# Kernel tuning notes

Hardware: AMD Instinct MI355X
Metric: run time of the kernel (lower is better)

Reference implementation:

```python
import jax, jax.numpy as jnp
import numpy as np

K_SIZE = 3
CH_IN = 256
NFILT = 256

def setup_inputs() -> dict:
    key = jax.random.key(0)
    k1, k2 = jax.random.split(key)
    x = jax.random.normal(k1, (32, 56, 56, CH_IN), dtype=jnp.float32)
    stdv = 1.0 / np.sqrt(K_SIZE * K_SIZE * CH_IN)
    w = jax.random.normal(k2, (K_SIZE, K_SIZE, CH_IN, NFILT), dtype=jnp.float32) * stdv
    pruning_mask = jnp.ones((K_SIZE * K_SIZE * CH_IN, NFILT), dtype=jnp.float32)
    return {"x": x, "w": w, "pruning_mask": pruning_mask}

def _magnitude_aware_weight(w):
    # scale = mean |w| over (kh, kw, cin), per output filter; stop-gradient
    scale = jax.lax.stop_gradient(jnp.mean(jnp.abs(w), axis=(0, 1, 2), keepdims=True))
    bw_no_grad = scale * jnp.sign(w)
    clipped = jnp.clip(w, -1.0, 1.0)
    # STE: forward = scale*sign(w), backward = d(clip(w,-1,1))
    return jax.lax.stop_gradient(bw_no_grad) - jax.lax.stop_gradient(clipped) + clipped

def reference(x, w, pruning_mask):
    kernel = _magnitude_aware_weight(w) * pruning_mask.reshape(K_SIZE, K_SIZE, CH_IN, NFILT)
    out = jax.lax.conv_general_dilated(
        x, kernel,
        window_strides=(1, 1),
        padding="SAME",
        dimension_numbers=("NHWC", "HWIO", "NHWC"),
    )
    return out
```

## Files before the change

### kernel.cpp

```cpp
#include <hip/hip_runtime.h>

typedef unsigned short u16;
typedef u16 u16x8 __attribute__((ext_vector_type(8)));
typedef __bf16 bf16x8 __attribute__((ext_vector_type(8)));
typedef float f32x4 __attribute__((ext_vector_type(4)));

#define NPIX 100352
#define KTOT 2304

static __device__ __forceinline__ u16 f2bf(float f) {
  unsigned u = __float_as_uint(f);
  return (u16)((u + 0x7fffu + ((u >> 16) & 1u)) >> 16);
}

static __device__ __forceinline__ bf16x8 as_bf(u16x8 v) {
  union { u16x8 u; bf16x8 b; } t; t.u = v; return t.b;
}

__global__ void scale_accum_k(const float* __restrict__ w, float* __restrict__ scale) {
  const int t = threadIdx.x;
  const long b = blockIdx.x;
  const float* p = w + b * 256 * 256 + t;
  float acc = 0.f;
#pragma unroll 8
  for (int e = 0; e < 256; ++e) acc += fabsf(p[(long)e * 256]);
  atomicAdd(&scale[t], acc);
}

__global__ void pack_w_k(const float* __restrict__ w, const float* __restrict__ mask,
                         const float* __restrict__ ssum, u16* __restrict__ wp) {
  __shared__ u16 t[128][33];
  const int k0 = blockIdx.x * 32;
  const int f0 = blockIdx.y * 128;
  const int tid = threadIdx.x;
#pragma unroll
  for (int i = 0; i < 16; ++i) {
    int idx = tid + i * 256;
    int kk = idx >> 7;
    int ff = idx & 127;
    long g = (long)(k0 + kk) * 256 + f0 + ff;
    float wv = w[g];
    float mv = mask[g];
    float sc = ssum[f0 + ff] * (1.0f / 2304.0f);
    float sg = (wv > 0.f) ? 1.f : ((wv < 0.f) ? -1.f : 0.f);
    t[ff][kk] = f2bf(sc * sg * mv);
  }
  __syncthreads();
#pragma unroll
  for (int i = 0; i < 8; ++i) {
    int idx = tid + i * 256;
    int row = idx >> 4;
    int c = idx & 15;
    unsigned v = (unsigned)t[row][2 * c] | ((unsigned)t[row][2 * c + 1] << 16);
    *(unsigned*)(wp + (long)(f0 + row) * KTOT + k0 + 2 * c) = v;
  }
}

__global__ void cvt_x_k(const float* __restrict__ x, u16* __restrict__ xb) {
  const long i = ((long)blockIdx.x * 256 + threadIdx.x) * 8;
  float4 a = *(const float4*)(x + i);
  float4 b = *(const float4*)(x + i + 4);
  u16x8 r;
  r[0] = f2bf(a.x); r[1] = f2bf(a.y); r[2] = f2bf(a.z); r[3] = f2bf(a.w);
  r[4] = f2bf(b.x); r[5] = f2bf(b.y); r[6] = f2bf(b.z); r[7] = f2bf(b.w);
  *(u16x8*)(xb + i) = r;
}

template <bool XB>
__global__ __launch_bounds__(256) void conv_gemm_k(
    const float* __restrict__ x, const u16* __restrict__ xb,
    const u16* __restrict__ wp, float* __restrict__ out) {
  __shared__ u16 As[128 * 40];
  __shared__ u16 Bs[128 * 40];

  const int tid = threadIdx.x;
  const int m0 = blockIdx.x * 128;
  const int n0 = blockIdx.y * 128;

  const int cc = tid & 3;
  const int r0 = tid >> 2;
  const int gm0 = m0 + r0;
  const int gm1 = gm0 + 64;
  const int pix0 = gm0 % 3136, oh0 = pix0 / 56, ow0 = pix0 % 56;
  const int pix1 = gm1 % 3136, oh1 = pix1 / 56, ow1 = pix1 % 56;

  const int lane = tid & 63;
  const int wv = tid >> 6;
  const int wm = wv & 1, wn = wv >> 1;
  const int lm = lane & 15, kq = lane >> 4;
  const int aoff = (wm * 64 + lm) * 40 + kq * 8;
  const int boff = (wn * 64 + lm) * 40 + kq * 8;

  u16* as0 = As + r0 * 40 + cc * 8;
  u16* as1 = As + (r0 + 64) * 40 + cc * 8;
  u16* bs0 = Bs + r0 * 40 + cc * 8;
  u16* bs1 = Bs + (r0 + 64) * 40 + cc * 8;

  const u16* wr0 = wp + (long)(n0 + r0) * KTOT + cc * 8;
  const u16* wr1 = wr0 + (long)64 * KTOT;

  f32x4 acc[4][4] = {};

  for (int khw = 0; khw < 9; ++khw) {
    const int dh = khw / 3 - 1;
    const int dw = khw % 3 - 1;
    const bool v0 = ((unsigned)(oh0 + dh) < 56u) && ((unsigned)(ow0 + dw) < 56u);
    const bool v1 = ((unsigned)(oh1 + dh) < 56u) && ((unsigned)(ow1 + dw) < 56u);
    const long p0 = ((long)gm0 + dh * 56 + dw) * 256 + cc * 8;
    const long p1 = ((long)gm1 + dh * 56 + dw) * 256 + cc * 8;
    const u16* wk0 = wr0 + khw * 256;
    const u16* wk1 = wr1 + khw * 256;

    for (int ct = 0; ct < 8; ++ct) {
      const int ci0 = ct * 32;
      u16x8 a0 = {0, 0, 0, 0, 0, 0, 0, 0};
      u16x8 a1 = {0, 0, 0, 0, 0, 0, 0, 0};
      if (XB) {
        if (v0) a0 = *(const u16x8*)(xb + p0 + ci0);
        if (v1) a1 = *(const u16x8*)(xb + p1 + ci0);
      } else {
        float4 l0 = make_float4(0, 0, 0, 0), h0 = make_float4(0, 0, 0, 0);
        float4 l1 = make_float4(0, 0, 0, 0), h1 = make_float4(0, 0, 0, 0);
        if (v0) { l0 = *(const float4*)(x + p0 + ci0); h0 = *(const float4*)(x + p0 + ci0 + 4); }
        if (v1) { l1 = *(const float4*)(x + p1 + ci0); h1 = *(const float4*)(x + p1 + ci0 + 4); }
        a0[0] = f2bf(l0.x); a0[1] = f2bf(l0.y); a0[2] = f2bf(l0.z); a0[3] = f2bf(l0.w);
        a0[4] = f2bf(h0.x); a0[5] = f2bf(h0.y); a0[6] = f2bf(h0.z); a0[7] = f2bf(h0.w);
        a1[0] = f2bf(l1.x); a1[1] = f2bf(l1.y); a1[2] = f2bf(l1.z); a1[3] = f2bf(l1.w);
        a1[4] = f2bf(h1.x); a1[5] = f2bf(h1.y); a1[6] = f2bf(h1.z); a1[7] = f2bf(h1.w);
      }
      u16x8 b0 = *(const u16x8*)(wk0 + ci0);
      u16x8 b1 = *(const u16x8*)(wk1 + ci0);

      __syncthreads();
      *(u16x8*)as0 = a0;
      *(u16x8*)as1 = a1;
      *(u16x8*)bs0 = b0;
      *(u16x8*)bs1 = b1;
      __syncthreads();

      bf16x8 av[4], bv[4];
#pragma unroll
      for (int i = 0; i < 4; ++i) av[i] = *(const bf16x8*)(As + aoff + i * 640);
#pragma unroll
      for (int i = 0; i < 4; ++i) bv[i] = *(const bf16x8*)(Bs + boff + i * 640);
#pragma unroll
      for (int mi = 0; mi < 4; ++mi) {
#pragma unroll
        for (int ni = 0; ni < 4; ++ni) {
          acc[mi][ni] = __builtin_amdgcn_mfma_f32_16x16x32_bf16(av[mi], bv[ni], acc[mi][ni], 0, 0, 0);
        }
      }
    }
  }

  float* op = out + (long)(m0 + wm * 64 + kq * 4) * 256 + n0 + wn * 64 + lm;
#pragma unroll
  for (int mi = 0; mi < 4; ++mi) {
#pragma unroll
    for (int ni = 0; ni < 4; ++ni) {
      float* p = op + (long)mi * 16 * 256 + ni * 16;
      f32x4 v = acc[mi][ni];
      p[0] = v[0];
      p[256] = v[1];
      p[512] = v[2];
      p[768] = v[3];
    }
  }
}

extern "C" void kernel_launch(void* const* d_in, const int* in_sizes, int n_in,
                              void* d_out, int out_size, void* d_ws, size_t ws_size,
                              hipStream_t stream) {
  const float* x = (const float*)d_in[0];
  const float* w = (const float*)d_in[1];
  const float* mask = (const float*)d_in[2];
  float* out = (float*)d_out;

  float* scale = (float*)d_ws;
  u16* wp = (u16*)((char*)d_ws + 1088);
  u16* xb = (u16*)((char*)d_ws + 1088 + 1179648);
  const size_t need = 1088 + 1179648 + (size_t)NPIX * 256 * 2;

  hipMemsetAsync(d_ws, 0, 1088, stream);
  scale_accum_k<<<9, 256, 0, stream>>>(w, scale);
  pack_w_k<<<dim3(72, 2), 256, 0, stream>>>(w, mask, scale, wp);
  if (ws_size >= need) {
    cvt_x_k<<<NPIX * 256 / (256 * 8), 256, 0, stream>>>(x, xb);
    conv_gemm_k<true><<<dim3(784, 2), 256, 0, stream>>>(x, xb, wp, out);
  } else {
    conv_gemm_k<false><<<dim3(784, 2), 256, 0, stream>>>(x, xb, wp, out);
  }
}
```

Baseline: 416.1 us.

## Pad input spatially and stream tiles into LDS with direct global-to-LDS loads

Converts the input to bf16 inside a zero-padded 58x58 per-image buffer, so the conv GEMM needs no boundary checks. The main kernel now uses global_load_lds to copy A and B tiles straight into LDS, with an XOR-swizzled unpadded layout to avoid bank conflicts, which removes the register round-trip. The weight-scale reduction is spread over more blocks. In exchange it adds a full memset of the padded buffer plus a scatter kernel, and relies on the 16-byte direct LDS load path and a larger workspace.

```diff
diff --git a/kernel.cpp b/kernel.cpp
--- a/kernel.cpp
+++ b/kernel.cpp
@@ -7,23 +7,25 @@
 
 #define NPIX 100352
 #define KTOT 2304
+#define IMG_PAD (58 * 58 * 256)
 
 static __device__ __forceinline__ u16 f2bf(float f) {
   unsigned u = __float_as_uint(f);
   return (u16)((u + 0x7fffu + ((u >> 16) & 1u)) >> 16);
 }
 
-static __device__ __forceinline__ bf16x8 as_bf(u16x8 v) {
-  union { u16x8 u; bf16x8 b; } t; t.u = v; return t.b;
+static __device__ __forceinline__ void gld_lds16(const u16* g, u16* l) {
+  __builtin_amdgcn_global_load_lds(
+      (const __attribute__((address_space(1))) void*)g,
+      (__attribute__((address_space(3))) void*)l, 16, 0, 0);
 }
 
 __global__ void scale_accum_k(const float* __restrict__ w, float* __restrict__ scale) {
   const int t = threadIdx.x;
-  const long b = blockIdx.x;
-  const float* p = w + b * 256 * 256 + t;
+  const float* p = w + (long)blockIdx.x * 64 * 256 + t;
   float acc = 0.f;
-#pragma unroll 8
-  for (int e = 0; e < 256; ++e) acc += fabsf(p[(long)e * 256]);
+#pragma unroll
+  for (int e = 0; e < 64; ++e) acc += fabsf(p[(long)e * 256]);
   atomicAdd(&scale[t], acc);
 }
 
@@ -56,51 +58,127 @@
   }
 }
 
-__global__ void cvt_x_k(const float* __restrict__ x, u16* __restrict__ xb) {
-  const long i = ((long)blockIdx.x * 256 + threadIdx.x) * 8;
-  float4 a = *(const float4*)(x + i);
-  float4 b = *(const float4*)(x + i + 4);
-  u16x8 r;
-  r[0] = f2bf(a.x); r[1] = f2bf(a.y); r[2] = f2bf(a.z); r[3] = f2bf(a.w);
-  r[4] = f2bf(b.x); r[5] = f2bf(b.y); r[6] = f2bf(b.z); r[7] = f2bf(b.w);
-  *(u16x8*)(xb + i) = r;
-}
-
-template <bool XB>
-__global__ __launch_bounds__(256) void conv_gemm_k(
-    const float* __restrict__ x, const u16* __restrict__ xb,
-    const u16* __restrict__ wp, float* __restrict__ out) {
+__global__ void fill_xpad_k(const float* __restrict__ x, u16* __restrict__ xp) {
+  const int tid = threadIdx.x;
+  const int pix = blockIdx.x * 8 + (tid >> 5);
+  const int c0 = (tid & 31) * 8;
+  const int img = pix / 3136;
+  const int r = pix % 3136;
+  const int oh = r / 56, ow = r % 56;
+  const float* s = x + (long)pix * 256 + c0;
+  float4 a = *(const float4*)s;
+  float4 b = *(const float4*)(s + 4);
+  u16x8 v;
+  v[0] = f2bf(a.x); v[1] = f2bf(a.y); v[2] = f2bf(a.z); v[3] = f2bf(a.w);
+  v[4] = f2bf(b.x); v[5] = f2bf(b.y); v[6] = f2bf(b.z); v[7] = f2bf(b.w);
+  *(u16x8*)(xp + (long)img * IMG_PAD + ((oh + 1) * 58 + ow + 1) * 256 + c0) = v;
+}
+
+__global__ __launch_bounds__(256) void conv_gemm2_k(
+    const u16* __restrict__ xpad, const u16* __restrict__ wp, float* __restrict__ out) {
+  __shared__ u16 As[128 * 32];
+  __shared__ u16 Bs[128 * 32];
+
+  const int tid = threadIdx.x;
+  const int lane = tid & 63;
+  const int wv = tid >> 6;
+  const int m0 = blockIdx.x * 128;
+  const int n0 = blockIdx.y * 128;
+
+  const int srow = lane >> 2;
+  const int cg = (lane & 3) ^ (srow & 3);
+  const int r0 = wv * 32 + srow;
+  const int r1 = r0 + 16;
+
+  const int gm0 = m0 + r0, gm1 = m0 + r1;
+  const int i0 = gm0 / 3136, q0 = gm0 % 3136;
+  const int i1 = gm1 / 3136, q1 = gm1 % 3136;
+  const u16* ap0 = xpad + (long)i0 * IMG_PAD + ((q0 / 56 + 1) * 58 + (q0 % 56) + 1) * 256 + cg * 8;
+  const u16* ap1 = xpad + (long)i1 * IMG_PAD + ((q1 / 56 + 1) * 58 + (q1 % 56) + 1) * 256 + cg * 8;
+  const u16* bp0 = wp + (long)(n0 + r0) * KTOT + cg * 8;
+  const u16* bp1 = wp + (long)(n0 + r1) * KTOT + cg * 8;
+
+  u16* asw0 = As + wv * 1024;
+  u16* asw1 = As + wv * 1024 + 512;
+  u16* bsw0 = Bs + wv * 1024;
+  u16* bsw1 = Bs + wv * 1024 + 512;
+
+  const int wm = wv & 1, wn = wv >> 1;
+  const int lm = lane & 15, kq = lane >> 4;
+  const int aoff = (wm * 64 + lm) * 32 + (kq ^ (lm & 3)) * 8;
+  const int boff = (wn * 64 + lm) * 32 + (kq ^ (lm & 3)) * 8;
+
+  f32x4 acc[4][4] = {};
+
+  for (int khw = 0; khw < 9; ++khw) {
+    const int dh = khw / 3 - 1, dw = khw % 3 - 1;
+    const int d = (dh * 58 + dw) * 256;
+    const u16* a0 = ap0 + d;
+    const u16* a1 = ap1 + d;
+    const u16* b0 = bp0 + khw * 256;
+    const u16* b1 = bp1 + khw * 256;
+#pragma unroll
+    for (int ct = 0; ct < 8; ++ct) {
+      gld_lds16(a0 + ct * 32, asw0);
+      gld_lds16(a1 + ct * 32, asw1);
+      gld_lds16(b0 + ct * 32, bsw0);
+      gld_lds16(b1 + ct * 32, bsw1);
+      __syncthreads();
+      bf16x8 av[4], bv[4];
+#pragma unroll
+      for (int i = 0; i < 4; ++i) av[i] = *(const bf16x8*)(As + aoff + i * 512);
+#pragma unroll
+      for (int i = 0; i < 4; ++i) bv[i] = *(const bf16x8*)(Bs + boff + i * 512);
+#pragma unroll
+      for (int mi = 0; mi < 4; ++mi)
+#pragma unroll
+        for (int ni = 0; ni < 4; ++ni)
+          acc[mi][ni] = __builtin_amdgcn_mfma_f32_16x16x32_bf16(av[mi], bv[ni], acc[mi][ni], 0, 0, 0);
+      __syncthreads();
+    }
+  }
+
+  float* op = out + (long)(m0 + wm * 64 + kq * 4) * 256 + n0 + wn * 64 + lm;
+#pragma unroll
+  for (int mi = 0; mi < 4; ++mi) {
+#pragma unroll
+    for (int ni = 0; ni < 4; ++ni) {
+      float* p = op + (long)mi * 16 * 256 + ni * 16;
+      f32x4 v = acc[mi][ni];
+      p[0] = v[0];
+      p[256] = v[1];
+      p[512] = v[2];
+      p[768] = v[3];
+    }
+  }
+}
+
+__global__ __launch_bounds__(256) void conv_gemm_fb_k(
+    const float* __restrict__ x, const u16* __restrict__ wp, float* __restrict__ out) {
   __shared__ u16 As[128 * 40];
   __shared__ u16 Bs[128 * 40];
-
   const int tid = threadIdx.x;
   const int m0 = blockIdx.x * 128;
   const int n0 = blockIdx.y * 128;
-
   const int cc = tid & 3;
   const int r0 = tid >> 2;
   const int gm0 = m0 + r0;
   const int gm1 = gm0 + 64;
   const int pix0 = gm0 % 3136, oh0 = pix0 / 56, ow0 = pix0 % 56;
   const int pix1 = gm1 % 3136, oh1 = pix1 / 56, ow1 = pix1 % 56;
-
   const int lane = tid & 63;
   const int wv = tid >> 6;
   const int wm = wv & 1, wn = wv >> 1;
   const int lm = lane & 15, kq = lane >> 4;
   const int aoff = (wm * 64 + lm) * 40 + kq * 8;
   const int boff = (wn * 64 + lm) * 40 + kq * 8;
-
   u16* as0 = As + r0 * 40 + cc * 8;
   u16* as1 = As + (r0 + 64) * 40 + cc * 8;
   u16* bs0 = Bs + r0 * 40 + cc * 8;
   u16* bs1 = Bs + (r0 + 64) * 40 + cc * 8;
-
   const u16* wr0 = wp + (long)(n0 + r0) * KTOT + cc * 8;
   const u16* wr1 = wr0 + (long)64 * KTOT;
-
   f32x4 acc[4][4] = {};
-
   for (int khw = 0; khw < 9; ++khw) {
     const int dh = khw / 3 - 1;
     const int dw = khw % 3 - 1;
@@ -110,62 +188,44 @@
     const long p1 = ((long)gm1 + dh * 56 + dw) * 256 + cc * 8;
     const u16* wk0 = wr0 + khw * 256;
     const u16* wk1 = wr1 + khw * 256;
-
     for (int ct = 0; ct < 8; ++ct) {
       const int ci0 = ct * 32;
-      u16x8 a0 = {0, 0, 0, 0, 0, 0, 0, 0};
-      u16x8 a1 = {0, 0, 0, 0, 0, 0, 0, 0};
-      if (XB) {
-        if (v0) a0 = *(const u16x8*)(xb + p0 + ci0);
-        if (v1) a1 = *(const u16x8*)(xb + p1 + ci0);
-      } else {
-        float4 l0 = make_float4(0, 0, 0, 0), h0 = make_float4(0, 0, 0, 0);
-        float4 l1 = make_float4(0, 0, 0, 0), h1 = make_float4(0, 0, 0, 0);
-        if (v0) { l0 = *(const float4*)(x + p0 + ci0); h0 = *(const float4*)(x + p0 + ci0 + 4); }
-        if (v1) { l1 = *(const float4*)(x + p1 + ci0); h1 = *(const float4*)(x + p1 + ci0 + 4); }
-        a0[0] = f2bf(l0.x); a0[1] = f2bf(l0.y); a0[2] = f2bf(l0.z); a0[3] = f2bf(l0.w);
-        a0[4] = f2bf(h0.x); a0[5] = f2bf(h0.y); a0[6] = f2bf(h0.z); a0[7] = f2bf(h0.w);
-        a1[0] = f2bf(l1.x); a1[1] = f2bf(l1.y); a1[2] = f2bf(l1.z); a1[3] = f2bf(l1.w);
-        a1[4] = f2bf(h1.x); a1[5] = f2bf(h1.y); a1[6] = f2bf(h1.z); a1[7] = f2bf(h1.w);
-      }
+      u16x8 a0 = {0,0,0,0,0,0,0,0}, a1 = {0,0,0,0,0,0,0,0};
+      float4 l0 = make_float4(0,0,0,0), h0 = make_float4(0,0,0,0);
+      float4 l1 = make_float4(0,0,0,0), h1 = make_float4(0,0,0,0);
+      if (v0) { l0 = *(const float4*)(x + p0 + ci0); h0 = *(const float4*)(x + p0 + ci0 + 4); }
+      if (v1) { l1 = *(const float4*)(x + p1 + ci0); h1 = *(const float4*)(x + p1 + ci0 + 4); }
+      a0[0]=f2bf(l0.x); a0[1]=f2bf(l0.y); a0[2]=f2bf(l0.z); a0[3]=f2bf(l0.w);
+      a0[4]=f2bf(h0.x); a0[5]=f2bf(h0.y); a0[6]=f2bf(h0.z); a0[7]=f2bf(h0.w);
+      a1[0]=f2bf(l1.x); a1[1]=f2bf(l1.y); a1[2]=f2bf(l1.z); a1[3]=f2bf(l1.w);
+      a1[4]=f2bf(h1.x); a1[5]=f2bf(h1.y); a1[6]=f2bf(h1.z); a1[7]=f2bf(h1.w);
       u16x8 b0 = *(const u16x8*)(wk0 + ci0);
       u16x8 b1 = *(const u16x8*)(wk1 + ci0);
-
-      __syncthreads();
-      *(u16x8*)as0 = a0;
-      *(u16x8*)as1 = a1;
-      *(u16x8*)bs0 = b0;
-      *(u16x8*)bs1 = b1;
-      __syncthreads();
-
+      __syncthreads();
+      *(u16x8*)as0 = a0; *(u16x8*)as1 = a1;
+      *(u16x8*)bs0 = b0; *(u16x8*)bs1 = b1;
+      __syncthreads();
       bf16x8 av[4], bv[4];
 #pragma unroll
       for (int i = 0; i < 4; ++i) av[i] = *(const bf16x8*)(As + aoff + i * 640);
 #pragma unroll
       for (int i = 0; i < 4; ++i) bv[i] = *(const bf16x8*)(Bs + boff + i * 640);
 #pragma unroll
-      for (int mi = 0; mi < 4; ++mi) {
-#pragma unroll
-        for (int ni = 0; ni < 4; ++ni) {
+      for (int mi = 0; mi < 4; ++mi)
+#pragma unroll
+        for (int ni = 0; ni < 4; ++ni)
           acc[mi][ni] = __builtin_amdgcn_mfma_f32_16x16x32_bf16(av[mi], bv[ni], acc[mi][ni], 0, 0, 0);
-        }
-      }
-    }
-  }
-
+    }
+  }
   float* op = out + (long)(m0 + wm * 64 + kq * 4) * 256 + n0 + wn * 64 + lm;
 #pragma unroll
-  for (int mi = 0; mi < 4; ++mi) {
+  for (int mi = 0; mi < 4; ++mi)
 #pragma unroll
     for (int ni = 0; ni < 4; ++ni) {
       float* p = op + (long)mi * 16 * 256 + ni * 16;
       f32x4 v = acc[mi][ni];
-      p[0] = v[0];
-      p[256] = v[1];
-      p[512] = v[2];
-      p[768] = v[3];
-    }
-  }
+      p[0] = v[0]; p[256] = v[1]; p[512] = v[2]; p[768] = v[3];
+    }
 }
 
 extern "C" void kernel_launch(void* const* d_in, const int* in_sizes, int n_in,
@@ -178,16 +238,18 @@
 
   float* scale = (float*)d_ws;
   u16* wp = (u16*)((char*)d_ws + 1088);
-  u16* xb = (u16*)((char*)d_ws + 1088 + 1179648);
-  const size_t need = 1088 + 1179648 + (size_t)NPIX * 256 * 2;
+  u16* xpad = (u16*)((char*)d_ws + 1088 + 1179648);
+  const size_t xpad_bytes = (size_t)32 * IMG_PAD * 2;
+  const size_t need = 1088 + 1179648 + xpad_bytes;
 
   hipMemsetAsync(d_ws, 0, 1088, stream);
-  scale_accum_k<<<9, 256, 0, stream>>>(w, scale);
+  scale_accum_k<<<36, 256, 0, stream>>>(w, scale);
   pack_w_k<<<dim3(72, 2), 256, 0, stream>>>(w, mask, scale, wp);
   if (ws_size >= need) {
-    cvt_x_k<<<NPIX * 256 / (256 * 8), 256, 0, stream>>>(x, xb);
-    conv_gemm_k<true><<<dim3(784, 2), 256, 0, stream>>>(x, xb, wp, out);
+    hipMemsetAsync(xpad, 0, xpad_bytes, stream);
+    fill_xpad_k<<<NPIX / 8, 256, 0, stream>>>(x, xpad);
+    conv_gemm2_k<<<dim3(784, 2), 256, 0, stream>>>(xpad, wp, out);
   } else {
-    conv_gemm_k<false><<<dim3(784, 2), 256, 0, stream>>>(x, xb, wp, out);
-  }
-}
+    conv_gemm_fb_k<<<dim3(784, 2), 256, 0, stream>>>(x, wp, out);
+  }
+}
```

Result: faster. 387.5 us (-6.9%).
